# Optimization experiments

Measured on AMD Instinct MI355X. Metric: run time of the kernel, lower is better.

## Reference

```python
import jax, jax.numpy as jnp
import numpy as np

B, S, D_IN = 16, 4096, 1024
H, HD = 8, 64            # num_heads, head_dim
V = H * HD               # value_dim = 512
F_OUT = 120              # forecast_horizon
EPS = 1e-5


def _rotate(x):
    # theta_shift in the source ignores sin/cos: stack((-x2, x1)) and flatten
    x1 = x[..., 0::2]
    x2 = x[..., 1::2]
    return jnp.stack((-x2, x1), axis=-1).reshape(x.shape)


def setup_inputs() -> dict:
    key = jax.random.key(0)
    kx, kq, kk, kv, ko, _ = jax.random.split(key, 6)
    return {
        "x": jax.random.normal(kx, (B, S, D_IN), dtype=jnp.float32),
        "Wq": jax.random.normal(kq, (V, D_IN), dtype=jnp.float32) * 0.02,
        "Wk": jax.random.normal(kk, (V, D_IN), dtype=jnp.float32) * 0.02,
        "Wv": jax.random.normal(kv, (V, D_IN), dtype=jnp.float32) * 0.02,
        "Wout": jax.random.normal(ko, (F_OUT, V), dtype=jnp.float32) * 0.02,
        "gamma": jnp.ones((V,), dtype=jnp.float32),  # RMSNorm weight
    }


def reference(x, Wq, Wk, Wv, Wout, gamma):
    b, s, _ = x.shape
    scaling = HD ** -0.5
    q = (x @ Wq.T) * scaling          # [B,S,V]
    k = (x @ Wk.T) * scaling
    v = (x @ Wv.T).reshape(b, H, s, HD)   # raw view reinterpretation (as in torch)
    qr = _rotate(q).reshape(b, H, s, HD)  # raw view, matches torch .view
    kr = _rotate(k).reshape(b, H, s, HD)
    # recurrent_forward with incremental_state=None:
    # kv = 0.9*0 + 0.1*(kr*v); output = sum_s(qr*kv); scale = S
    kv = 0.1 * (kr * v)
    out = jnp.sum(qr * kv, axis=2) / jnp.float32(s)  # [B,H,HD]
    out = out.reshape(b, H * HD)                      # [B,V]
    # RMSNorm
    rms = out * jax.lax.rsqrt(jnp.mean(out * out, axis=-1, keepdims=True) + EPS) * gamma
    g = jax.nn.gelu(rms, approximate=False)  # torch F.gelu default = exact erf
    return g @ Wout.T                         # [B, forecast_horizon]
```

## Files before the change

kernel.cpp:

```cpp
#include <hip/hip_runtime.h>
#include <hip/hip_bf16.h>
#include <math.h>

#define B_   16
#define S_   4096
#define DIN  1024
#define V_   512
#define FOUT 120

typedef __attribute__((ext_vector_type(8))) short bf16x8;
typedef __attribute__((ext_vector_type(4))) float f32x4;

#define AS1 __attribute__((address_space(1)))
#define AS3 __attribute__((address_space(3)))

__device__ const float CSCALE = 0.1f / (64.0f * 4096.0f);
__device__ const float EPSF = 1e-5f;

__device__ inline void gl2lds16(const void* g, void* l) {
  __builtin_amdgcn_global_load_lds((const AS1 unsigned int*)g,
                                   (AS3 unsigned int*)l, 16, 0, 0);
}

__device__ inline unsigned short f2b(float f) {
  unsigned u = __builtin_bit_cast(unsigned, f);
  unsigned r = (u + 0x7FFFu + ((u >> 16) & 1u)) >> 16;
  return (unsigned short)r;
}

__device__ inline bf16x8 pack8(float4 a, float4 b) {
  bf16x8 r;
  r[0] = (short)f2b(a.x); r[1] = (short)f2b(a.y);
  r[2] = (short)f2b(a.z); r[3] = (short)f2b(a.w);
  r[4] = (short)f2b(b.x); r[5] = (short)f2b(b.y);
  r[6] = (short)f2b(b.z); r[7] = (short)f2b(b.w);
  return r;
}

__global__ void msr_convw(const float* __restrict__ Wq, const float* __restrict__ Wk,
                          const float* __restrict__ Wv, unsigned short* __restrict__ Wt) {
  int e = blockIdx.x * 256 + threadIdx.x;
  int l = e & 63;
  int f = (e >> 6) % 24;
  int ck = (e >> 6) / 24;
  int k = ck & 31;
  int ct = ck >> 5;
  int nf = f / 3, g = f % 3;
  const float* W = (g == 0) ? Wq : (g == 1) ? Wk : Wv;
  int ch = ct * 128 + nf * 16 + (l & 15);
  const float* src = W + (size_t)ch * DIN + k * 32 + (l >> 4) * 8;
  float4 a = *(const float4*)src;
  float4 b = *(const float4*)(src + 4);
  *(bf16x8*)(Wt + (size_t)e * 8) = pack8(a, b);
}

__global__ __launch_bounds__(256) void msr_convx(const float* __restrict__ x,
                                                 unsigned short* __restrict__ Xb) {
  const size_t stride = (size_t)gridDim.x * 256;
  for (size_t i = blockIdx.x * 256ull + threadIdx.x; i < 8388608ull; i += stride) {
    const float* src = x + i * 8;
    float4 a = *(const float4*)src;
    float4 b = *(const float4*)(src + 4);
    *(bf16x8*)(Xb + i * 8) = pack8(a, b);
  }
}

#define WAITVM4  asm volatile("s_waitcnt vmcnt(4)" ::: "memory")
#define WAITVM0  asm volatile("s_waitcnt vmcnt(0)" ::: "memory")
#define WAITLGKM asm volatile("s_waitcnt lgkmcnt(0)" ::: "memory")
#define SCHEDB   __builtin_amdgcn_sched_barrier(0)
#define BARRIER  { asm volatile("" ::: "memory"); __builtin_amdgcn_s_barrier(); asm volatile("" ::: "memory"); }

template <bool DIRECT>
__global__ __launch_bounds__(512, 2) void msr_main(
    const float* __restrict__ x, const unsigned short* __restrict__ Xb,
    const unsigned short* __restrict__ Wt, float* __restrict__ outacc) {
  const int bid = blockIdx.x;
  const int ct = bid & 3;
  const int rt = bid >> 2;
  const int r0 = rt << 7;

  __shared__ __align__(16) unsigned char smem_[98304];

  const int t = threadIdx.x;
  const int w = t >> 6, lane = t & 63;
  const int wm4 = (w >> 2) * 4;
  const int l16 = lane * 16;
  const int w3 = w * 3;
  const int ctk = ct * 32;
  const int bread = 8192 + 6 * (w & 3) * 1024 + l16;

  const unsigned short* pXs = Xb + (size_t)(r0 + w * 16 + (lane & 15)) * DIN + ((lane >> 4) << 3);

  const int awoff = ((((t >> 2) >> 4) * 64) + (t & 3) * 16 + ((t >> 2) & 15)) * 16;
  const float* pXf = x + (size_t)(r0 + (t >> 2)) * DIN + (t & 3) * 8;

  f32x4 acc[3][4][2];
#pragma unroll
  for (int g = 0; g < 3; ++g)
#pragma unroll
    for (int m = 0; m < 4; ++m)
#pragma unroll
      for (int n = 0; n < 2; ++n) acc[g][m][n] = (f32x4){0.f, 0.f, 0.f, 0.f};

  bf16x8 afr[4], bfr0[3], bfr1[3];

#define STAGE(KK, SB) { \
  if (DIRECT) { \
    gl2lds16(pXs + (size_t)(KK) * 32, smem_ + (SB) * 32768 + w * 1024); \
  } else { \
    const float* p = pXf + (size_t)(KK) * 32; \
    *(bf16x8*)(smem_ + (SB) * 32768 + awoff) = pack8(*(const float4*)p, *(const float4*)(p + 4)); \
  } \
  _Pragma("unroll") for (int i = 0; i < 3; ++i) \
    gl2lds16(Wt + ((size_t)(ctk + (KK)) * 24 + w3 + i) * 512 + (size_t)lane * 8, \
             smem_ + (SB) * 32768 + 8192 + (w3 + i) * 1024); }

#define READS(KB) { \
  _Pragma("unroll") for (int m = 0; m < 4; ++m) \
    afr[m] = *(const bf16x8*)(smem_ + (KB) * 32768 + (wm4 + m) * 1024 + l16); \
  _Pragma("unroll") for (int g = 0; g < 3; ++g) \
    bfr0[g] = *(const bf16x8*)(smem_ + (KB) * 32768 + bread + g * 1024); \
  _Pragma("unroll") for (int g = 0; g < 3; ++g) \
    bfr1[g] = *(const bf16x8*)(smem_ + (KB) * 32768 + bread + 3072 + g * 1024); }

#define MFMAP(NN, BFR) { \
  __builtin_amdgcn_s_setprio(1); \
  _Pragma("unroll") for (int g = 0; g < 3; ++g) \
  _Pragma("unroll") for (int m = 0; m < 4; ++m) \
    acc[g][m][NN] = __builtin_amdgcn_mfma_f32_16x16x32_bf16(afr[m], BFR[g], acc[g][m][NN], 0, 0, 0); \
  __builtin_amdgcn_s_setprio(0); }

#define STEP(KB, SB, KK, DOSTAGE, VMW) { \
  READS(KB); \
  if (DOSTAGE) { STAGE((KK) + 2, SB); } \
  SCHEDB; \
  MFMAP(0, bfr0); \
  MFMAP(1, bfr1); \
  if (!DIRECT) { WAITLGKM; } \
  VMW; \
  BARRIER; }

  STAGE(0, 0);
  STAGE(1, 1);
  if (!DIRECT) { WAITLGKM; }
  WAITVM4;
  BARRIER;

#pragma unroll 1
  for (int i = 0; i < 10; ++i) {
    const int k3 = i * 3;
    STEP(0, 2, k3,     1, WAITVM4);
    STEP(1, 0, k3 + 1, 1, WAITVM4);
    STEP(2, 1, k3 + 2, 1, WAITVM4);
  }
  STEP(0, 0, 30, 0, WAITVM0);
  READS(1);
  MFMAP(0, bfr0);
  MFMAP(1, bfr1);
#undef STEP
#undef MFMAP
#undef READS
#undef STAGE

  float pd0 = 0.f, pd1 = 0.f;
#pragma unroll
  for (int m = 0; m < 4; ++m)
#pragma unroll
    for (int r = 0; r < 4; ++r) {
      float qk0 = acc[0][m][0][r] * acc[1][m][0][r];
      float qk1 = acc[0][m][1][r] * acc[1][m][1][r];
      pd0 += __shfl_xor(qk0, 1, 64) * acc[2][m][0][r];
      pd1 += __shfl_xor(qk1, 1, 64) * acc[2][m][1][r];
    }
  pd0 += __shfl_xor(pd0, 16, 64); pd0 += __shfl_xor(pd0, 32, 64);
  pd1 += __shfl_xor(pd1, 16, 64); pd1 += __shfl_xor(pd1, 32, 64);

  if (lane < 16) {
    float* dst = &outacc[((rt >> 2) << 6) + (w & 1) * 32 + lane];
    atomicAdd(dst, pd0);
    atomicAdd(dst + 16, pd1);
  }
}

__global__ __launch_bounds__(256) void msr_finish(
    const float* __restrict__ outacc, const float* __restrict__ gamma,
    const float* __restrict__ Wout, float* __restrict__ y) {
  const int b = blockIdx.x;
  const int t = threadIdx.x;
  __shared__ float g[V_];
  __shared__ float wsum[4];

  float v0 = outacc[b * V_ + t] * CSCALE;
  float v1 = outacc[b * V_ + 256 + t] * CSCALE;
  float ss = v0 * v0 + v1 * v1;
#pragma unroll
  for (int o = 32; o > 0; o >>= 1) ss += __shfl_down(ss, o, 64);
  if ((t & 63) == 0) wsum[t >> 6] = ss;
  __syncthreads();
  float tot = wsum[0] + wsum[1] + wsum[2] + wsum[3];
  float rs = rsqrtf(tot * (1.0f / (float)V_) + EPSF);

  float r0v = v0 * rs * gamma[t];
  float r1v = v1 * rs * gamma[t + 256];
  g[t]       = 0.5f * r0v * (1.0f + erff(r0v * 0.70710678118654752f));
  g[t + 256] = 0.5f * r1v * (1.0f + erff(r1v * 0.70710678118654752f));
  __syncthreads();

  if (t < FOUT) {
    const float* wr = Wout + (size_t)t * V_;
    float acc = 0.f;
#pragma unroll 4
    for (int c = 0; c < V_; c += 4) {
      float4 w4 = *(const float4*)(wr + c);
      acc += g[c] * w4.x + g[c + 1] * w4.y + g[c + 2] * w4.z + g[c + 3] * w4.w;
    }
    y[b * FOUT + t] = acc;
  }
}

extern "C" void kernel_launch(void* const* d_in, const int* in_sizes, int n_in,
                              void* d_out, int out_size, void* d_ws, size_t ws_size,
                              hipStream_t stream) {
  const float* x     = (const float*)d_in[0];
  const float* Wq    = (const float*)d_in[1];
  const float* Wk    = (const float*)d_in[2];
  const float* Wv    = (const float*)d_in[3];
  const float* Wout  = (const float*)d_in[4];
  const float* gamma = (const float*)d_in[5];

  float* outacc = (float*)d_ws;
  unsigned short* Wt = (unsigned short*)((char*)d_ws + 32768);
  unsigned short* Xb = (unsigned short*)((char*)d_ws + 32768 + 3145728);
  float* y = (float*)d_out;

  const size_t need = 32768ull + 3145728ull + 134217728ull;

  msr_convw<<<768, 256, 0, stream>>>(Wq, Wk, Wv, Wt);
  hipMemsetAsync(outacc, 0, B_ * V_ * sizeof(float), stream);

  if (ws_size >= need) {
    msr_convx<<<2048, 256, 0, stream>>>(x, Xb);
    msr_main<true><<<2048, 512, 0, stream>>>(x, Xb, Wt, outacc);
  } else {
    msr_main<false><<<2048, 512, 0, stream>>>(x, Xb, Wt, outacc);
  }
  msr_finish<<<B_, 256, 0, stream>>>(outacc, gamma, Wout, y);
}
```

Measured before the change: 269.7 us.

## Shrink main GEMM tile to 64 rows with register-staged A and XCD-aware block mapping

The main fused QKV kernel now uses 256-thread blocks over 64-row tiles, which doubles the grid to 4096 blocks. Block IDs are remapped so consecutive blocks on the same XCD share row tiles. X fragments are loaded into registers with inline global loads and written to a double-buffered LDS slot one step later, while each wave stages six weight fragments through direct-to-LDS loads. This aims to improve latency hiding and L2 locality, at the cost of reloading the weight tile twice as often per row and more hand-tuned waitcnt bookkeeping that could be fragile.

```diff
diff --git a/kernel.cpp b/kernel.cpp
--- a/kernel.cpp
+++ b/kernel.cpp
@@ -65,35 +65,35 @@
   }
 }
 
-#define WAITVM4  asm volatile("s_waitcnt vmcnt(4)" ::: "memory")
+#define WAITVM7  asm volatile("s_waitcnt vmcnt(7)" ::: "memory")
 #define WAITVM0  asm volatile("s_waitcnt vmcnt(0)" ::: "memory")
 #define WAITLGKM asm volatile("s_waitcnt lgkmcnt(0)" ::: "memory")
 #define SCHEDB   __builtin_amdgcn_sched_barrier(0)
 #define BARRIER  { asm volatile("" ::: "memory"); __builtin_amdgcn_s_barrier(); asm volatile("" ::: "memory"); }
 
 template <bool DIRECT>
-__global__ __launch_bounds__(512, 2) void msr_main(
+__global__ __launch_bounds__(256, 2) void msr_main(
     const float* __restrict__ x, const unsigned short* __restrict__ Xb,
     const unsigned short* __restrict__ Wt, float* __restrict__ outacc) {
   const int bid = blockIdx.x;
-  const int ct = bid & 3;
-  const int rt = bid >> 2;
-  const int r0 = rt << 7;
-
-  __shared__ __align__(16) unsigned char smem_[98304];
+  const int xcd = bid & 7;
+  const int j = bid >> 3;
+  const int ct = j & 3;
+  const int rt = xcd * 128 + (j >> 2);
+  const int r0 = rt << 6;
+
+  __shared__ __align__(16) unsigned char smem_[81920];
 
   const int t = threadIdx.x;
   const int w = t >> 6, lane = t & 63;
-  const int wm4 = (w >> 2) * 4;
+  const int w6 = w * 6;
   const int l16 = lane * 16;
-  const int w3 = w * 3;
-  const int ctk = ct * 32;
-  const int bread = 8192 + 6 * (w & 3) * 1024 + l16;
-
-  const unsigned short* pXs = Xb + (size_t)(r0 + w * 16 + (lane & 15)) * DIN + ((lane >> 4) << 3);
-
-  const int awoff = ((((t >> 2) >> 4) * 64) + (t & 3) * 16 + ((t >> 2) & 15)) * 16;
+
+  const unsigned short* pWt =
+      Wt + (((size_t)ct * 32) * 24 + w6) * 512 + (size_t)lane * 8;
+  const unsigned short* pXa = Xb + (size_t)(r0 + (t >> 2)) * DIN + (t & 3) * 8;
   const float* pXf = x + (size_t)(r0 + (t >> 2)) * DIN + (t & 3) * 8;
+  const int awoff = (((t >> 2) >> 4) * 64 + (t & 3) * 16 + ((t >> 2) & 15)) * 16;
 
   f32x4 acc[3][4][2];
 #pragma unroll
@@ -104,64 +104,89 @@
       for (int n = 0; n < 2; ++n) acc[g][m][n] = (f32x4){0.f, 0.f, 0.f, 0.f};
 
   bf16x8 afr[4], bfr0[3], bfr1[3];
-
-#define STAGE(KK, SB) { \
-  if (DIRECT) { \
-    gl2lds16(pXs + (size_t)(KK) * 32, smem_ + (SB) * 32768 + w * 1024); \
+  bf16x8 xE, xO;
+
+#define ALOAD(REG, PX, PXF, C2) { \
+  if constexpr (DIRECT) { \
+    const unsigned short* _p = (PX) + (size_t)(C2) * 32; \
+    asm volatile("global_load_dwordx4 %0, %1, off" : "=v"(REG) : "v"(_p) : "memory"); \
   } else { \
-    const float* p = pXf + (size_t)(KK) * 32; \
-    *(bf16x8*)(smem_ + (SB) * 32768 + awoff) = pack8(*(const float4*)p, *(const float4*)(p + 4)); \
-  } \
-  _Pragma("unroll") for (int i = 0; i < 3; ++i) \
-    gl2lds16(Wt + ((size_t)(ctk + (KK)) * 24 + w3 + i) * 512 + (size_t)lane * 8, \
-             smem_ + (SB) * 32768 + 8192 + (w3 + i) * 1024); }
-
-#define READS(KB) { \
+    const float* _pf = (PXF) + (size_t)(C2) * 32; \
+    REG = pack8(*(const float4*)_pf, *(const float4*)(_pf + 4)); \
+  } }
+
+#define STAGEB(PW, C2, SB) { \
+  _Pragma("unroll") for (int i = 0; i < 6; ++i) \
+    gl2lds16((PW) + (size_t)(C2) * 12288 + i * 512, \
+             smem_ + 8192 + (SB) * 24576 + (w6 + i) * 1024); }
+
+#define READS(KB, AB) { \
   _Pragma("unroll") for (int m = 0; m < 4; ++m) \
-    afr[m] = *(const bf16x8*)(smem_ + (KB) * 32768 + (wm4 + m) * 1024 + l16); \
+    afr[m] = *(const bf16x8*)(smem_ + (AB) * 4096 + (m * 64 + lane) * 16); \
   _Pragma("unroll") for (int g = 0; g < 3; ++g) \
-    bfr0[g] = *(const bf16x8*)(smem_ + (KB) * 32768 + bread + g * 1024); \
+    bfr0[g] = *(const bf16x8*)(smem_ + 8192 + (KB) * 24576 + (w6 + g) * 1024 + l16); \
   _Pragma("unroll") for (int g = 0; g < 3; ++g) \
-    bfr1[g] = *(const bf16x8*)(smem_ + (KB) * 32768 + bread + 3072 + g * 1024); }
-
-#define MFMAP(NN, BFR) { \
+    bfr1[g] = *(const bf16x8*)(smem_ + 8192 + (KB) * 24576 + (w6 + 3 + g) * 1024 + l16); }
+
+#define MFMAP { \
   __builtin_amdgcn_s_setprio(1); \
   _Pragma("unroll") for (int g = 0; g < 3; ++g) \
-  _Pragma("unroll") for (int m = 0; m < 4; ++m) \
-    acc[g][m][NN] = __builtin_amdgcn_mfma_f32_16x16x32_bf16(afr[m], BFR[g], acc[g][m][NN], 0, 0, 0); \
+  _Pragma("unroll") for (int m = 0; m < 4; ++m) { \
+    acc[g][m][0] = __builtin_amdgcn_mfma_f32_16x16x32_bf16(afr[m], bfr0[g], acc[g][m][0], 0, 0, 0); \
+    acc[g][m][1] = __builtin_amdgcn_mfma_f32_16x16x32_bf16(afr[m], bfr1[g], acc[g][m][1], 0, 0, 0); \
+  } \
   __builtin_amdgcn_s_setprio(0); }
 
-#define STEP(KB, SB, KK, DOSTAGE, VMW) { \
-  READS(KB); \
-  if (DOSTAGE) { STAGE((KK) + 2, SB); } \
+#define STEP(KB, AB, SB, C2, REGW, REGL) { \
+  READS(KB, AB); \
+  STAGEB(pWi, C2, SB); \
+  ALOAD(REGL, pXi, pXfi, C2); \
   SCHEDB; \
-  MFMAP(0, bfr0); \
-  MFMAP(1, bfr1); \
-  if (!DIRECT) { WAITLGKM; } \
-  VMW; \
+  MFMAP; \
+  WAITVM7; \
+  *(bf16x8*)(smem_ + ((AB) ^ 1) * 4096 + awoff) = REGW; \
+  WAITLGKM; \
   BARRIER; }
 
-  STAGE(0, 0);
-  STAGE(1, 1);
-  if (!DIRECT) { WAITLGKM; }
-  WAITVM4;
+  ALOAD(xE, pXa, pXf, 0);
+  STAGEB(pWt, 0, 0);
+  STAGEB(pWt, 1, 1);
+  ALOAD(xO, pXa, pXf, 1);
+  if constexpr (DIRECT) { asm volatile("s_waitcnt vmcnt(13)" ::: "memory"); }
+  *(bf16x8*)(smem_ + awoff) = xE;
+  WAITVM7;
+  WAITLGKM;
   BARRIER;
 
+  const unsigned short* pWi = pWt;
+  const unsigned short* pXi = pXa;
+  const float* pXfi = pXf;
 #pragma unroll 1
-  for (int i = 0; i < 10; ++i) {
-    const int k3 = i * 3;
-    STEP(0, 2, k3,     1, WAITVM4);
-    STEP(1, 0, k3 + 1, 1, WAITVM4);
-    STEP(2, 1, k3 + 2, 1, WAITVM4);
-  }
-  STEP(0, 0, 30, 0, WAITVM0);
-  READS(1);
-  MFMAP(0, bfr0);
-  MFMAP(1, bfr1);
+  for (int i = 0; i < 5; ++i) {
+    STEP(0, 0, 2, 2, xO, xE);
+    STEP(1, 1, 0, 3, xE, xO);
+    STEP(2, 0, 1, 4, xO, xE);
+    STEP(0, 1, 2, 5, xE, xO);
+    STEP(1, 0, 0, 6, xO, xE);
+    STEP(2, 1, 1, 7, xE, xO);
+    pWi += 6 * 12288;
+    pXi += 6 * 32;
+    pXfi += 6 * 32;
+  }
+  READS(0, 0);
+  SCHEDB;
+  MFMAP;
+  WAITVM0;
+  *(bf16x8*)(smem_ + 4096 + awoff) = xO;
+  WAITLGKM;
+  BARRIER;
+  READS(1, 1);
+  MFMAP;
 #undef STEP
 #undef MFMAP
 #undef READS
-#undef STAGE
+#undef STAGEB
+#undef ALOAD
 
   float pd0 = 0.f, pd1 = 0.f;
 #pragma unroll
@@ -177,7 +202,7 @@
   pd1 += __shfl_xor(pd1, 16, 64); pd1 += __shfl_xor(pd1, 32, 64);
 
   if (lane < 16) {
-    float* dst = &outacc[((rt >> 2) << 6) + (w & 1) * 32 + lane];
+    float* dst = &outacc[((rt >> 3) << 6) + (w & 1) * 32 + lane];
     atomicAdd(dst, pd0);
     atomicAdd(dst + 16, pd1);
   }
@@ -241,9 +266,9 @@
 
   if (ws_size >= need) {
     msr_convx<<<2048, 256, 0, stream>>>(x, Xb);
-    msr_main<true><<<2048, 512, 0, stream>>>(x, Xb, Wt, outacc);
+    msr_main<true><<<4096, 256, 0, stream>>>(x, Xb, Wt, outacc);
   } else {
-    msr_main<false><<<2048, 512, 0, stream>>>(x, Xb, Wt, outacc);
+    msr_main<false><<<4096, 256, 0, stream>>>(x, Xb, Wt, outacc);
   }
   msr_finish<<<B_, 256, 0, stream>>>(outacc, gamma, Wout, y);
 }
```

New measurement: 301.3 us. 1.12x slower.

## Drop separate x->bf16 pass; stream fp32 x into LDS and convert at read

Applied to the files above, without the earlier changes.

Removes the msr_convx pre-pass that wrote a 128 MB bf16 copy of x. The main kernel now loads fp32 x tiles straight into LDS with global_load_lds and packs them to bf16 when reading fragments. It also remaps block IDs so each XCD handles a contiguous range of row tiles, which should help L2 reuse across the four column tiles. In exchange, the larger LDS footprint (120 KB) drops occupancy to one block per CU, and every column-tile block re-reads fp32 x at twice the bytes and repeats the conversion work.

```diff
diff --git a/kernel.cpp b/kernel.cpp
--- a/kernel.cpp
+++ b/kernel.cpp
@@ -54,33 +54,21 @@
   *(bf16x8*)(Wt + (size_t)e * 8) = pack8(a, b);
 }
 
-__global__ __launch_bounds__(256) void msr_convx(const float* __restrict__ x,
-                                                 unsigned short* __restrict__ Xb) {
-  const size_t stride = (size_t)gridDim.x * 256;
-  for (size_t i = blockIdx.x * 256ull + threadIdx.x; i < 8388608ull; i += stride) {
-    const float* src = x + i * 8;
-    float4 a = *(const float4*)src;
-    float4 b = *(const float4*)(src + 4);
-    *(bf16x8*)(Xb + i * 8) = pack8(a, b);
-  }
-}
-
-#define WAITVM4  asm volatile("s_waitcnt vmcnt(4)" ::: "memory")
-#define WAITVM0  asm volatile("s_waitcnt vmcnt(0)" ::: "memory")
-#define WAITLGKM asm volatile("s_waitcnt lgkmcnt(0)" ::: "memory")
-#define SCHEDB   __builtin_amdgcn_sched_barrier(0)
-#define BARRIER  { asm volatile("" ::: "memory"); __builtin_amdgcn_s_barrier(); asm volatile("" ::: "memory"); }
-
-template <bool DIRECT>
-__global__ __launch_bounds__(512, 2) void msr_main(
-    const float* __restrict__ x, const unsigned short* __restrict__ Xb,
-    const unsigned short* __restrict__ Wt, float* __restrict__ outacc) {
+#define WAITVM5 asm volatile("s_waitcnt vmcnt(5)" ::: "memory")
+#define WAITVM0 asm volatile("s_waitcnt vmcnt(0)" ::: "memory")
+#define BARRIER { asm volatile("" ::: "memory"); __builtin_amdgcn_s_barrier(); asm volatile("" ::: "memory"); }
+
+__global__ __launch_bounds__(512, 1) void msr_main(
+    const float* __restrict__ x, const unsigned short* __restrict__ Wt,
+    float* __restrict__ outacc) {
   const int bid = blockIdx.x;
-  const int ct = bid & 3;
-  const int rt = bid >> 2;
+  const int xcd = bid & 7;
+  const int j = bid >> 3;
+  const int ct = j & 3;
+  const int rt = xcd * 64 + (j >> 2);
   const int r0 = rt << 7;
 
-  __shared__ __align__(16) unsigned char smem_[98304];
+  __shared__ __align__(16) unsigned char smem_[122880];
 
   const int t = threadIdx.x;
   const int w = t >> 6, lane = t & 63;
@@ -88,12 +76,13 @@
   const int l16 = lane * 16;
   const int w3 = w * 3;
   const int ctk = ct * 32;
-  const int bread = 8192 + 6 * (w & 3) * 1024 + l16;
-
-  const unsigned short* pXs = Xb + (size_t)(r0 + w * 16 + (lane & 15)) * DIN + ((lane >> 4) << 3);
-
-  const int awoff = ((((t >> 2) >> 4) * 64) + (t & 3) * 16 + ((t >> 2) & 15)) * 16;
-  const float* pXf = x + (size_t)(r0 + (t >> 2)) * DIN + (t & 3) * 8;
+  const int bread = 16384 + 6 * (w & 3) * 1024 + l16;
+
+  const float* srcA0 = x + (size_t)(r0 + (w >> 1) * 16 + (lane & 15)) * DIN
+                         + ((lane >> 4) << 3) + (w & 1) * 4;
+  const float* srcA1 = srcA0 + (size_t)64 * DIN;
+  const int dA0 = w * 1024;
+  const int dA1 = (8 + w) * 1024;
 
   f32x4 acc[3][4][2];
 #pragma unroll
@@ -106,58 +95,56 @@
   bf16x8 afr[4], bfr0[3], bfr1[3];
 
 #define STAGE(KK, SB) { \
-  if (DIRECT) { \
-    gl2lds16(pXs + (size_t)(KK) * 32, smem_ + (SB) * 32768 + w * 1024); \
-  } else { \
-    const float* p = pXf + (size_t)(KK) * 32; \
-    *(bf16x8*)(smem_ + (SB) * 32768 + awoff) = pack8(*(const float4*)p, *(const float4*)(p + 4)); \
-  } \
+  unsigned char* _sb = smem_ + (SB) * 40960; \
+  gl2lds16(srcA0 + (size_t)(KK) * 32, _sb + dA0); \
+  gl2lds16(srcA1 + (size_t)(KK) * 32, _sb + dA1); \
   _Pragma("unroll") for (int i = 0; i < 3; ++i) \
     gl2lds16(Wt + ((size_t)(ctk + (KK)) * 24 + w3 + i) * 512 + (size_t)lane * 8, \
-             smem_ + (SB) * 32768 + 8192 + (w3 + i) * 1024); }
+             _sb + 16384 + (w3 + i) * 1024); }
 
 #define READS(KB) { \
-  _Pragma("unroll") for (int m = 0; m < 4; ++m) \
-    afr[m] = *(const bf16x8*)(smem_ + (KB) * 32768 + (wm4 + m) * 1024 + l16); \
+  const unsigned char* _kb = smem_ + (KB) * 40960; \
+  _Pragma("unroll") for (int m = 0; m < 4; ++m) { \
+    float4 _f0 = *(const float4*)(_kb + (wm4 + m) * 2048 + l16); \
+    float4 _f1 = *(const float4*)(_kb + (wm4 + m) * 2048 + 1024 + l16); \
+    afr[m] = pack8(_f0, _f1); \
+  } \
   _Pragma("unroll") for (int g = 0; g < 3; ++g) \
-    bfr0[g] = *(const bf16x8*)(smem_ + (KB) * 32768 + bread + g * 1024); \
+    bfr0[g] = *(const bf16x8*)(_kb + bread + g * 1024); \
   _Pragma("unroll") for (int g = 0; g < 3; ++g) \
-    bfr1[g] = *(const bf16x8*)(smem_ + (KB) * 32768 + bread + 3072 + g * 1024); }
-
-#define MFMAP(NN, BFR) { \
+    bfr1[g] = *(const bf16x8*)(_kb + bread + 3072 + g * 1024); }
+
+#define MFMAP { \
   __builtin_amdgcn_s_setprio(1); \
   _Pragma("unroll") for (int g = 0; g < 3; ++g) \
-  _Pragma("unroll") for (int m = 0; m < 4; ++m) \
-    acc[g][m][NN] = __builtin_amdgcn_mfma_f32_16x16x32_bf16(afr[m], BFR[g], acc[g][m][NN], 0, 0, 0); \
+  _Pragma("unroll") for (int m = 0; m < 4; ++m) { \
+    acc[g][m][0] = __builtin_amdgcn_mfma_f32_16x16x32_bf16(afr[m], bfr0[g], acc[g][m][0], 0, 0, 0); \
+    acc[g][m][1] = __builtin_amdgcn_mfma_f32_16x16x32_bf16(afr[m], bfr1[g], acc[g][m][1], 0, 0, 0); \
+  } \
   __builtin_amdgcn_s_setprio(0); }
 
 #define STEP(KB, SB, KK, DOSTAGE, VMW) { \
   READS(KB); \
   if (DOSTAGE) { STAGE((KK) + 2, SB); } \
-  SCHEDB; \
-  MFMAP(0, bfr0); \
-  MFMAP(1, bfr1); \
-  if (!DIRECT) { WAITLGKM; } \
+  MFMAP; \
   VMW; \
   BARRIER; }
 
   STAGE(0, 0);
   STAGE(1, 1);
-  if (!DIRECT) { WAITLGKM; }
-  WAITVM4;
+  WAITVM5;
   BARRIER;
 
 #pragma unroll 1
   for (int i = 0; i < 10; ++i) {
     const int k3 = i * 3;
-    STEP(0, 2, k3,     1, WAITVM4);
-    STEP(1, 0, k3 + 1, 1, WAITVM4);
-    STEP(2, 1, k3 + 2, 1, WAITVM4);
+    STEP(0, 2, k3,     1, WAITVM5);
+    STEP(1, 0, k3 + 1, 1, WAITVM5);
+    STEP(2, 1, k3 + 2, 1, WAITVM5);
   }
   STEP(0, 0, 30, 0, WAITVM0);
   READS(1);
-  MFMAP(0, bfr0);
-  MFMAP(1, bfr1);
+  MFMAP;
 #undef STEP
 #undef MFMAP
 #undef READS
@@ -231,19 +218,10 @@
 
   float* outacc = (float*)d_ws;
   unsigned short* Wt = (unsigned short*)((char*)d_ws + 32768);
-  unsigned short* Xb = (unsigned short*)((char*)d_ws + 32768 + 3145728);
   float* y = (float*)d_out;
-
-  const size_t need = 32768ull + 3145728ull + 134217728ull;
 
   msr_convw<<<768, 256, 0, stream>>>(Wq, Wk, Wv, Wt);
   hipMemsetAsync(outacc, 0, B_ * V_ * sizeof(float), stream);
-
-  if (ws_size >= need) {
-    msr_convx<<<2048, 256, 0, stream>>>(x, Xb);
-    msr_main<true><<<2048, 512, 0, stream>>>(x, Xb, Wt, outacc);
-  } else {
-    msr_main<false><<<2048, 512, 0, stream>>>(x, Xb, Wt, outacc);
-  }
+  msr_main<<<2048, 512, 0, stream>>>(x, Wt, outacc);
   msr_finish<<<B_, 256, 0, stream>>>(outacc, gamma, Wout, y);
 }
```

New measurement: 277.8 us. 3.0% more time.

## Double the row tile to 256 per block and swizzle blocks across XCDs

Applied to the files above, without the earlier changes.

Each block now computes 256 rows instead of 128, so every wave holds 8 M-fragments and the grid halves to 1024 blocks. Each staged weight tile is reused across twice as many rows, which cuts weight LDS traffic and global reloads per output. Blocks are remapped so that consecutive row tiles land on the same XCD for L2 locality, and the MFMA loop now interleaves A-fragment reads with the MFMAs. The cost is more accumulator registers (96 f32x4), more LDS (120KB), and a `__launch_bounds__(512, 2)` that can no longer be met given that LDS, so occupancy likely drops to one block per CU.

```diff
diff --git a/kernel.cpp b/kernel.cpp
--- a/kernel.cpp
+++ b/kernel.cpp
@@ -65,10 +65,10 @@
   }
 }
 
-#define WAITVM4  asm volatile("s_waitcnt vmcnt(4)" ::: "memory")
+#define WAITVM5  asm volatile("s_waitcnt vmcnt(5)" ::: "memory")
+#define WAITVM3  asm volatile("s_waitcnt vmcnt(3)" ::: "memory")
 #define WAITVM0  asm volatile("s_waitcnt vmcnt(0)" ::: "memory")
 #define WAITLGKM asm volatile("s_waitcnt lgkmcnt(0)" ::: "memory")
-#define SCHEDB   __builtin_amdgcn_sched_barrier(0)
 #define BARRIER  { asm volatile("" ::: "memory"); __builtin_amdgcn_s_barrier(); asm volatile("" ::: "memory"); }
 
 template <bool DIRECT>
@@ -76,96 +76,94 @@
     const float* __restrict__ x, const unsigned short* __restrict__ Xb,
     const unsigned short* __restrict__ Wt, float* __restrict__ outacc) {
   const int bid = blockIdx.x;
-  const int ct = bid & 3;
-  const int rt = bid >> 2;
-  const int r0 = rt << 7;
-
-  __shared__ __align__(16) unsigned char smem_[98304];
+  const int xcd = bid & 7;
+  const int j = bid >> 3;
+  const int ct = j & 3;
+  const int rt = xcd * 32 + (j >> 2);
+  const int r0 = rt << 8;
+
+  __shared__ __align__(16) unsigned char smem_[122880];
 
   const int t = threadIdx.x;
   const int w = t >> 6, lane = t & 63;
-  const int wm4 = (w >> 2) * 4;
   const int l16 = lane * 16;
   const int w3 = w * 3;
   const int ctk = ct * 32;
-  const int bread = 8192 + 6 * (w & 3) * 1024 + l16;
-
-  const unsigned short* pXs = Xb + (size_t)(r0 + w * 16 + (lane & 15)) * DIN + ((lane >> 4) << 3);
-
-  const int awoff = ((((t >> 2) >> 4) * 64) + (t & 3) * 16 + ((t >> 2) & 15)) * 16;
-  const float* pXf = x + (size_t)(r0 + (t >> 2)) * DIN + (t & 3) * 8;
-
-  f32x4 acc[3][4][2];
+  const int amb = (w >> 2) * 8192;
+  const int bread = 16384 + 6 * (w & 3) * 1024 + l16;
+
+  const unsigned short* srcA0 =
+      Xb + (size_t)(r0 + w * 16 + (lane & 15)) * DIN + ((lane >> 4) << 3);
+  const unsigned short* srcA1 = srcA0 + (size_t)128 * DIN;
+  const float* pXf = x + (size_t)(r0 + w * 16 + (lane & 15)) * DIN + ((lane >> 4) << 3);
+
+  f32x4 acc[3][8][2];
 #pragma unroll
   for (int g = 0; g < 3; ++g)
 #pragma unroll
-    for (int m = 0; m < 4; ++m)
+    for (int m = 0; m < 8; ++m)
 #pragma unroll
       for (int n = 0; n < 2; ++n) acc[g][m][n] = (f32x4){0.f, 0.f, 0.f, 0.f};
 
-  bf16x8 afr[4], bfr0[3], bfr1[3];
-
 #define STAGE(KK, SB) { \
-  if (DIRECT) { \
-    gl2lds16(pXs + (size_t)(KK) * 32, smem_ + (SB) * 32768 + w * 1024); \
+  unsigned char* _sb = smem_ + (SB) * 40960; \
+  if constexpr (DIRECT) { \
+    gl2lds16(srcA0 + (size_t)(KK) * 32, _sb + w * 1024); \
+    gl2lds16(srcA1 + (size_t)(KK) * 32, _sb + (8 + w) * 1024); \
   } else { \
-    const float* p = pXf + (size_t)(KK) * 32; \
-    *(bf16x8*)(smem_ + (SB) * 32768 + awoff) = pack8(*(const float4*)p, *(const float4*)(p + 4)); \
+    const float* _p0 = pXf + (size_t)(KK) * 32; \
+    const float* _p1 = _p0 + (size_t)128 * DIN; \
+    *(bf16x8*)(_sb + (w * 64 + lane) * 16) = \
+        pack8(*(const float4*)_p0, *(const float4*)(_p0 + 4)); \
+    *(bf16x8*)(_sb + ((8 + w) * 64 + lane) * 16) = \
+        pack8(*(const float4*)_p1, *(const float4*)(_p1 + 4)); \
   } \
   _Pragma("unroll") for (int i = 0; i < 3; ++i) \
     gl2lds16(Wt + ((size_t)(ctk + (KK)) * 24 + w3 + i) * 512 + (size_t)lane * 8, \
-             smem_ + (SB) * 32768 + 8192 + (w3 + i) * 1024); }
-
-#define READS(KB) { \
-  _Pragma("unroll") for (int m = 0; m < 4; ++m) \
-    afr[m] = *(const bf16x8*)(smem_ + (KB) * 32768 + (wm4 + m) * 1024 + l16); \
-  _Pragma("unroll") for (int g = 0; g < 3; ++g) \
-    bfr0[g] = *(const bf16x8*)(smem_ + (KB) * 32768 + bread + g * 1024); \
-  _Pragma("unroll") for (int g = 0; g < 3; ++g) \
-    bfr1[g] = *(const bf16x8*)(smem_ + (KB) * 32768 + bread + 3072 + g * 1024); }
-
-#define MFMAP(NN, BFR) { \
+             _sb + 16384 + (w3 + i) * 1024); }
+
+#define COMPUTE(KB) { \
+  const unsigned char* _kb = smem_ + (KB) * 40960; \
+  bf16x8 _bfr[6]; \
+  _Pragma("unroll") for (int i = 0; i < 6; ++i) \
+    _bfr[i] = *(const bf16x8*)(_kb + bread + i * 1024); \
   __builtin_amdgcn_s_setprio(1); \
-  _Pragma("unroll") for (int g = 0; g < 3; ++g) \
-  _Pragma("unroll") for (int m = 0; m < 4; ++m) \
-    acc[g][m][NN] = __builtin_amdgcn_mfma_f32_16x16x32_bf16(afr[m], BFR[g], acc[g][m][NN], 0, 0, 0); \
+  _Pragma("unroll") for (int m = 0; m < 8; ++m) { \
+    bf16x8 _afr = *(const bf16x8*)(_kb + amb + m * 1024 + l16); \
+    _Pragma("unroll") for (int g = 0; g < 3; ++g) { \
+      acc[g][m][0] = __builtin_amdgcn_mfma_f32_16x16x32_bf16(_afr, _bfr[g],     acc[g][m][0], 0, 0, 0); \
+      acc[g][m][1] = __builtin_amdgcn_mfma_f32_16x16x32_bf16(_afr, _bfr[3 + g], acc[g][m][1], 0, 0, 0); \
+    } \
+  } \
   __builtin_amdgcn_s_setprio(0); }
 
-#define STEP(KB, SB, KK, DOSTAGE, VMW) { \
-  READS(KB); \
+#define STEP(KB, SB, KK, DOSTAGE, VMD, VMF) { \
   if (DOSTAGE) { STAGE((KK) + 2, SB); } \
-  SCHEDB; \
-  MFMAP(0, bfr0); \
-  MFMAP(1, bfr1); \
-  if (!DIRECT) { WAITLGKM; } \
-  VMW; \
+  COMPUTE(KB); \
+  if constexpr (DIRECT) { VMD; } else { WAITLGKM; VMF; } \
   BARRIER; }
 
   STAGE(0, 0);
   STAGE(1, 1);
-  if (!DIRECT) { WAITLGKM; }
-  WAITVM4;
+  if constexpr (DIRECT) { WAITVM5; } else { WAITLGKM; WAITVM3; }
   BARRIER;
 
 #pragma unroll 1
   for (int i = 0; i < 10; ++i) {
     const int k3 = i * 3;
-    STEP(0, 2, k3,     1, WAITVM4);
-    STEP(1, 0, k3 + 1, 1, WAITVM4);
-    STEP(2, 1, k3 + 2, 1, WAITVM4);
-  }
-  STEP(0, 0, 30, 0, WAITVM0);
-  READS(1);
-  MFMAP(0, bfr0);
-  MFMAP(1, bfr1);
+    STEP(0, 2, k3,     1, WAITVM5, WAITVM3);
+    STEP(1, 0, k3 + 1, 1, WAITVM5, WAITVM3);
+    STEP(2, 1, k3 + 2, 1, WAITVM5, WAITVM3);
+  }
+  STEP(0, 0, 30, 0, WAITVM0, WAITVM0);
+  COMPUTE(1);
 #undef STEP
-#undef MFMAP
-#undef READS
+#undef COMPUTE
 #undef STAGE
 
   float pd0 = 0.f, pd1 = 0.f;
 #pragma unroll
-  for (int m = 0; m < 4; ++m)
+  for (int m = 0; m < 8; ++m)
 #pragma unroll
     for (int r = 0; r < 4; ++r) {
       float qk0 = acc[0][m][0][r] * acc[1][m][0][r];
@@ -177,7 +175,7 @@
   pd1 += __shfl_xor(pd1, 16, 64); pd1 += __shfl_xor(pd1, 32, 64);
 
   if (lane < 16) {
-    float* dst = &outacc[((rt >> 2) << 6) + (w & 1) * 32 + lane];
+    float* dst = &outacc[((rt >> 1) << 6) + (w & 1) * 32 + lane];
     atomicAdd(dst, pd0);
     atomicAdd(dst + 16, pd1);
   }
@@ -241,9 +239,9 @@
 
   if (ws_size >= need) {
     msr_convx<<<2048, 256, 0, stream>>>(x, Xb);
-    msr_main<true><<<2048, 512, 0, stream>>>(x, Xb, Wt, outacc);
+    msr_main<true><<<1024, 512, 0, stream>>>(x, Xb, Wt, outacc);
   } else {
-    msr_main<false><<<2048, 512, 0, stream>>>(x, Xb, Wt, outacc);
+    msr_main<false><<<1024, 512, 0, stream>>>(x, Xb, Wt, outacc);
   }
   msr_finish<<<B_, 256, 0, stream>>>(outacc, gamma, Wout, y);
 }
```

Measured after the change: 255.3 us. -5.3%, faster.
